# Performance work log

Measured on AMD Instinct MI355X. Metric: run time of the kernel, lower is better.

The kernel has to match this reference:

```python
import jax, jax.numpy as jnp
import numpy as np

N, D, H, E = 50000, 128, 512, 500000

def setup_inputs() -> dict:
    key = jax.random.key(0)
    k1, k2, k3, k4 = jax.random.split(key, 4)
    z = jax.random.normal(k1, (N, D), dtype=jnp.float32)
    edge_index = jax.random.randint(k2, (2, E), 0, N, dtype=jnp.int64)
    # torch Linear weights: fc1 [H, 2D], fc2 [1, H]
    W1 = jax.random.normal(k3, (H, 2 * D), dtype=jnp.float32) * (1.0 / np.sqrt(2 * D))
    b1 = jnp.zeros((H,), dtype=jnp.float32)
    W2 = jax.random.normal(k4, (1, H), dtype=jnp.float32) * (1.0 / np.sqrt(H))
    b2 = jnp.zeros((1,), dtype=jnp.float32)
    return {"z": z, "edge_index": edge_index, "W1": W1, "b1": b1, "W2": W2, "b2": b2}

def reference(z, edge_index, W1, b1, W2, b2):
    # gather endpoints and concat along feature dim: [E, 2D]
    z_cat = jnp.concatenate([z[edge_index[0]], z[edge_index[1]]], axis=1)
    # dropout is identity at eval (drop_rate effectively 0 for the baseline)
    h = jax.nn.relu(jnp.einsum('ef,hf->eh', z_cat, W1) + b1)  # [E, H]
    y = (jnp.einsum('eh,oh->eo', h, W2) + b2).reshape(-1)     # [E]
    return y
```

## Files before the change

kernel.cpp:

```cpp
#include <hip/hip_runtime.h>


typedef __bf16 bf16x8 __attribute__((ext_vector_type(8)));
typedef float f32x4 __attribute__((ext_vector_type(4)));

__device__ __forceinline__ unsigned short f2b(float f) {
    unsigned int u = __float_as_uint(f);
    u = (u + 0x7fffu + ((u >> 16) & 1u)) >> 16;
    return (unsigned short)u;
}

__device__ __forceinline__ void gload_lds16(const unsigned short* g, unsigned short* l) {
    __builtin_amdgcn_global_load_lds(
        (const __attribute__((address_space(1))) unsigned int*)g,
        (__attribute__((address_space(3))) unsigned int*)l, 16, 0, 0);
}

__global__ void prep_kernel(const float* __restrict__ z, const float* __restrict__ W1,
                            const float* __restrict__ b2p,
                            unsigned short* __restrict__ zb, unsigned short* __restrict__ w1s,
                            float* __restrict__ outz, int nz4, int nout4) {
    int stride = gridDim.x * blockDim.x;
    const int nw = 256 * 64;
    const int total = nz4 + nw + nout4;
    const float b2v = b2p[0];
    for (int idx = blockIdx.x * blockDim.x + threadIdx.x; idx < total; idx += stride) {
        if (idx < nz4) {
            float4 v = ((const float4*)z)[idx];
            ushort4 o;
            o.x = f2b(v.x); o.y = f2b(v.y); o.z = f2b(v.z); o.w = f2b(v.w);
            ((ushort4*)zb)[idx] = o;
        } else if (idx < nz4 + nw) {
            int u = idx - nz4;
            int lane = u & 63;
            int blk  = u >> 6;
            int h  = (blk >> 3) * 16 + (lane & 15);
            int kb = (blk & 7) * 32 + (lane >> 4) * 8;
            const float* src = W1 + h * 256 + kb;
            ushort4 o0, o1;
            float4 v0 = *(const float4*)(src);
            float4 v1 = *(const float4*)(src + 4);
            o0.x = f2b(v0.x); o0.y = f2b(v0.y); o0.z = f2b(v0.z); o0.w = f2b(v0.w);
            o1.x = f2b(v1.x); o1.y = f2b(v1.y); o1.z = f2b(v1.z); o1.w = f2b(v1.w);
            ushort4* dst = (ushort4*)(w1s + u * 8);
            dst[0] = o0; dst[1] = o1;
        } else {
            ((float4*)outz)[idx - nz4 - nw] = (float4){b2v, b2v, b2v, b2v};
        }
    }
}

__global__ __launch_bounds__(512, 2)
void edge_mlp_kernel(const int* __restrict__ ei, const unsigned short* __restrict__ zb,
                     const unsigned short* __restrict__ w1s,
                     const float* __restrict__ b1, const float* __restrict__ W2,
                     float* __restrict__ out, int E, int ntiles) {
    __shared__ unsigned short ldsA[2][64 * 256];
    __shared__ float ldsB1[512];

    const int tid  = threadIdx.x;
    const int lane = tid & 63;
    const int w    = tid >> 6;
    const int l15  = lane & 15;
    const int l4   = lane >> 4;
    const int G    = gridDim.x;
    const int t0   = blockIdx.x;
    if (t0 >= ntiles) return;

    ldsB1[tid] = b1[tid];

    uint4 breg[4][8];
    #pragma unroll
    for (int j = 0; j < 4; ++j)
        #pragma unroll
        for (int kc = 0; kc < 8; ++kc)
            breg[j][kc] = *(const uint4*)(w1s + (((w * 4 + j) * 8 + kc) << 9) + lane * 8);

    f32x4 w2v[4];
    #pragma unroll
    for (int j = 0; j < 4; ++j)
        w2v[j] = *(const f32x4*)&W2[w * 64 + j * 16 + l4 * 4];

    const int side = (lane >> 4) & 1;
    const int rsub = lane >> 5;
    const int swz  = l15 & 7;

#define ISSUE_GATHER(BUF)                                                     \
    do {                                                                      \
        _Pragma("unroll")                                                     \
        for (int q_ = 0; q_ < 4; ++q_) {                                      \
            int m_   = w * 8 + q_ * 2 + rsub;                                 \
            int s15_ = l15 ^ (m_ & 7);                                        \
            gload_lds16(zb + (((long)ival[q_]) << 7) + (s15_ << 3),           \
                        &ldsA[BUF][(w * 8 + q_ * 2) << 8]);                   \
        }                                                                     \
    } while (0)

    asm volatile("s_waitcnt vmcnt(0) lgkmcnt(0)" ::: "memory");

    int ival[4];
    #pragma unroll
    for (int q = 0; q < 4; ++q) {
        int e = t0 * 64 + w * 8 + q * 2 + rsub;
        e = (e < E) ? e : (E - 1);
        ival[q] = ei[side * E + e];
    }
    ISSUE_GATHER(0);
    asm volatile("" ::: "memory");
    {
        int t1 = t0 + G;
        #pragma unroll
        for (int q = 0; q < 4; ++q) {
            int e = t1 * 64 + w * 8 + q * 2 + rsub;
            e = (e < E) ? e : (E - 1);
            ival[q] = ei[side * E + e];
        }
    }
    asm volatile("" ::: "memory");
    if (l4 == 0) {
        #pragma unroll
        for (int i = 0; i < 4; ++i)
            atomicAdd(&out[t0 * 64 + i * 16 + l15], 0.0f);
    }

    int cur = 0;
    for (int t = t0; t < ntiles; t += G) {
        asm volatile("s_waitcnt vmcnt(8)" ::: "memory");
        __builtin_amdgcn_s_barrier();
        asm volatile("" ::: "memory");

        const unsigned short* bufc = &ldsA[cur][0];

        f32x4 acc[4][4];
        {
            f32x4 b1t[4];
            #pragma unroll
            for (int j = 0; j < 4; ++j)
                b1t[j] = *(const f32x4*)&ldsB1[w * 64 + j * 16 + l4 * 4];
            #pragma unroll
            for (int i = 0; i < 4; i++)
                #pragma unroll
                for (int j = 0; j < 4; j++) acc[i][j] = b1t[j];
        }

        __builtin_amdgcn_s_setprio(1);
        #pragma unroll
        for (int kc = 0; kc < 4; ++kc) {
            bf16x8 a[4];
            #pragma unroll
            for (int i = 0; i < 4; ++i)
                a[i] = *(const bf16x8*)&bufc[((l15 + 16 * i) << 8) + ((((kc << 2) + l4) ^ swz) << 3)];
            #pragma unroll
            for (int i = 0; i < 4; ++i)
                #pragma unroll
                for (int j = 0; j < 4; ++j)
                    acc[i][j] = __builtin_amdgcn_mfma_f32_16x16x32_bf16(
                        *(const bf16x8*)&breg[j][kc], a[i], acc[i][j], 0, 0, 0);
        }
        __builtin_amdgcn_s_setprio(0);

        ISSUE_GATHER(cur ^ 1);
        asm volatile("" ::: "memory");

        __builtin_amdgcn_s_setprio(1);
        #pragma unroll
        for (int kc = 4; kc < 8; ++kc) {
            bf16x8 a[4];
            #pragma unroll
            for (int i = 0; i < 4; ++i)
                a[i] = *(const bf16x8*)&bufc[((l15 + 16 * i) << 8) + ((((kc << 2) + l4) ^ swz) << 3)];
            #pragma unroll
            for (int i = 0; i < 4; ++i)
                #pragma unroll
                for (int j = 0; j < 4; ++j)
                    acc[i][j] = __builtin_amdgcn_mfma_f32_16x16x32_bf16(
                        *(const bf16x8*)&breg[j][kc], a[i], acc[i][j], 0, 0, 0);
        }
        __builtin_amdgcn_s_setprio(0);

        {
            int tt = t + 2 * G;
            #pragma unroll
            for (int q = 0; q < 4; ++q) {
                int e = tt * 64 + w * 8 + q * 2 + rsub;
                e = (e < E) ? e : (E - 1);
                ival[q] = ei[side * E + e];
            }
        }
        asm volatile("" ::: "memory");

        float s4[4];
        #pragma unroll
        for (int i = 0; i < 4; i++) {
            float s = 0.f;
            #pragma unroll
            for (int j = 0; j < 4; j++)
                #pragma unroll
                for (int r = 0; r < 4; r++)
                    s = fmaf(fmaxf(acc[i][j][r], 0.f), w2v[j][r], s);
            s += __shfl_xor(s, 16);
            s += __shfl_xor(s, 32);
            s4[i] = s;
        }
        #pragma unroll
        for (int i = 0; i < 4; i++) {
            int e = t * 64 + i * 16 + l15;
            if (l4 == 0 && e < E) atomicAdd(&out[e], s4[i]);
        }

        cur ^= 1;
    }
#undef ISSUE_GATHER
}

extern "C" void kernel_launch(void* const* d_in, const int* in_sizes, int n_in,
                              void* d_out, int out_size, void* d_ws, size_t ws_size,
                              hipStream_t stream) {
    const float* z  = (const float*)d_in[0];
    const int*   ei = (const int*)d_in[1];
    const float* W1 = (const float*)d_in[2];
    const float* b1 = (const float*)d_in[3];
    const float* W2 = (const float*)d_in[4];
    const float* b2 = (const float*)d_in[5];
    float* out = (float*)d_out;

    const int E  = in_sizes[1] / 2;
    const int NZ = in_sizes[0];

    unsigned short* zb  = (unsigned short*)d_ws;
    unsigned short* w1s = zb + NZ;

    prep_kernel<<<2048, 256, 0, stream>>>(z, W1, b2, zb, w1s, out, NZ / 4, E / 4);

    const int ntiles = (E + 63) / 64;
    int grid = 256;
    edge_mlp_kernel<<<grid, 512, 0, stream>>>(ei, zb, w1s, b1, W2, out, E, ntiles);
}
```

Before: 182.8 us.

## Fuse bf16 prep pass into edge MLP kernel via cooperative grid sync

```diff
diff --git a/kernel.cpp b/kernel.cpp
--- a/kernel.cpp
+++ b/kernel.cpp
@@ -1,4 +1,7 @@
 #include <hip/hip_runtime.h>
+#include <hip/hip_cooperative_groups.h>
+
+namespace cg = cooperative_groups;
 
 
 typedef __bf16 bf16x8 __attribute__((ext_vector_type(8)));
@@ -16,45 +19,12 @@
         (__attribute__((address_space(3))) unsigned int*)l, 16, 0, 0);
 }
 
-__global__ void prep_kernel(const float* __restrict__ z, const float* __restrict__ W1,
-                            const float* __restrict__ b2p,
-                            unsigned short* __restrict__ zb, unsigned short* __restrict__ w1s,
-                            float* __restrict__ outz, int nz4, int nout4) {
-    int stride = gridDim.x * blockDim.x;
-    const int nw = 256 * 64;
-    const int total = nz4 + nw + nout4;
-    const float b2v = b2p[0];
-    for (int idx = blockIdx.x * blockDim.x + threadIdx.x; idx < total; idx += stride) {
-        if (idx < nz4) {
-            float4 v = ((const float4*)z)[idx];
-            ushort4 o;
-            o.x = f2b(v.x); o.y = f2b(v.y); o.z = f2b(v.z); o.w = f2b(v.w);
-            ((ushort4*)zb)[idx] = o;
-        } else if (idx < nz4 + nw) {
-            int u = idx - nz4;
-            int lane = u & 63;
-            int blk  = u >> 6;
-            int h  = (blk >> 3) * 16 + (lane & 15);
-            int kb = (blk & 7) * 32 + (lane >> 4) * 8;
-            const float* src = W1 + h * 256 + kb;
-            ushort4 o0, o1;
-            float4 v0 = *(const float4*)(src);
-            float4 v1 = *(const float4*)(src + 4);
-            o0.x = f2b(v0.x); o0.y = f2b(v0.y); o0.z = f2b(v0.z); o0.w = f2b(v0.w);
-            o1.x = f2b(v1.x); o1.y = f2b(v1.y); o1.z = f2b(v1.z); o1.w = f2b(v1.w);
-            ushort4* dst = (ushort4*)(w1s + u * 8);
-            dst[0] = o0; dst[1] = o1;
-        } else {
-            ((float4*)outz)[idx - nz4 - nw] = (float4){b2v, b2v, b2v, b2v};
-        }
-    }
-}
-
 __global__ __launch_bounds__(512, 2)
-void edge_mlp_kernel(const int* __restrict__ ei, const unsigned short* __restrict__ zb,
-                     const unsigned short* __restrict__ w1s,
-                     const float* __restrict__ b1, const float* __restrict__ W2,
-                     float* __restrict__ out, int E, int ntiles) {
+void fused_kernel(const float* __restrict__ z, const int* __restrict__ ei,
+                  const float* __restrict__ W1, const float* __restrict__ b1,
+                  const float* __restrict__ W2, const float* __restrict__ b2p,
+                  unsigned short* __restrict__ zb, unsigned short* __restrict__ w1s,
+                  float* __restrict__ out, int E, int NZ, int ntiles) {
     __shared__ unsigned short ldsA[2][64 * 256];
     __shared__ float ldsB1[512];
 
@@ -65,9 +35,42 @@
     const int l4   = lane >> 4;
     const int G    = gridDim.x;
     const int t0   = blockIdx.x;
-    if (t0 >= ntiles) return;
-
-    ldsB1[tid] = b1[tid];
+
+    {
+        const int nz4   = NZ / 4;
+        const int nw    = 256 * 64;
+        const int nout4 = E / 4;
+        const int total = nz4 + nw + nout4;
+        const int stride = G * 512;
+        const float b2v = b2p[0];
+        for (int idx = t0 * 512 + tid; idx < total; idx += stride) {
+            if (idx < nz4) {
+                float4 v = ((const float4*)z)[idx];
+                ushort4 o;
+                o.x = f2b(v.x); o.y = f2b(v.y); o.z = f2b(v.z); o.w = f2b(v.w);
+                ((ushort4*)zb)[idx] = o;
+            } else if (idx < nz4 + nw) {
+                int u = idx - nz4;
+                int ln = u & 63;
+                int blk  = u >> 6;
+                int h  = (blk >> 3) * 16 + (ln & 15);
+                int kb = (blk & 7) * 32 + (ln >> 4) * 8;
+                const float* src = W1 + h * 256 + kb;
+                ushort4 o0, o1;
+                float4 v0 = *(const float4*)(src);
+                float4 v1 = *(const float4*)(src + 4);
+                o0.x = f2b(v0.x); o0.y = f2b(v0.y); o0.z = f2b(v0.z); o0.w = f2b(v0.w);
+                o1.x = f2b(v1.x); o1.y = f2b(v1.y); o1.z = f2b(v1.z); o1.w = f2b(v1.w);
+                ushort4* dst = (ushort4*)(w1s + u * 8);
+                dst[0] = o0; dst[1] = o1;
+            } else {
+                ((float4*)out)[idx - nz4 - nw] = (float4){b2v, b2v, b2v, b2v};
+            }
+        }
+        ldsB1[tid] = b1[tid];
+    }
+
+    cg::this_grid().sync();
 
     uint4 breg[4][8];
     #pragma unroll
@@ -224,15 +227,17 @@
     const float* b2 = (const float*)d_in[5];
     float* out = (float*)d_out;
 
-    const int E  = in_sizes[1] / 2;
-    const int NZ = in_sizes[0];
+    int E  = in_sizes[1] / 2;
+    int NZ = in_sizes[0];
 
     unsigned short* zb  = (unsigned short*)d_ws;
     unsigned short* w1s = zb + NZ;
 
-    prep_kernel<<<2048, 256, 0, stream>>>(z, W1, b2, zb, w1s, out, NZ / 4, E / 4);
-
-    const int ntiles = (E + 63) / 64;
-    int grid = 256;
-    edge_mlp_kernel<<<grid, 512, 0, stream>>>(ei, zb, w1s, b1, W2, out, E, ntiles);
-}
+    int ntiles = (E + 63) / 64;
+
+    void* args[] = { (void*)&z, (void*)&ei, (void*)&W1, (void*)&b1,
+                     (void*)&W2, (void*)&b2, (void*)&zb, (void*)&w1s,
+                     (void*)&out, (void*)&E, (void*)&NZ, (void*)&ntiles };
+    hipLaunchCooperativeKernel((const void*)fused_kernel,
+                               dim3(256), dim3(512), args, 0, stream);
+}
```

Result: slower. 234.4 us (+28.2%).

## Switch edge MLP GEMM from 16x16x32 to 32x32x16 bf16 MFMA tiles

Applied to the files above, without the earlier changes.

```diff
diff --git a/kernel.cpp b/kernel.cpp
--- a/kernel.cpp
+++ b/kernel.cpp
@@ -2,7 +2,8 @@
 
 
 typedef __bf16 bf16x8 __attribute__((ext_vector_type(8)));
-typedef float f32x4 __attribute__((ext_vector_type(4)));
+typedef float f32x4  __attribute__((ext_vector_type(4)));
+typedef float f32x16 __attribute__((ext_vector_type(16)));
 
 __device__ __forceinline__ unsigned short f2b(float f) {
     unsigned int u = __float_as_uint(f);
@@ -34,8 +35,8 @@
             int u = idx - nz4;
             int lane = u & 63;
             int blk  = u >> 6;
-            int h  = (blk >> 3) * 16 + (lane & 15);
-            int kb = (blk & 7) * 32 + (lane >> 4) * 8;
+            int h  = (blk >> 4) * 32 + (lane & 31);
+            int kb = (blk & 15) * 16 + (lane >> 5) * 8;
             const float* src = W1 + h * 256 + kb;
             ushort4 o0, o1;
             float4 v0 = *(const float4*)(src);
@@ -57,39 +58,36 @@
                      float* __restrict__ out, int E, int ntiles) {
     __shared__ unsigned short ldsA[2][64 * 256];
     __shared__ float ldsB1[512];
+    __shared__ float ldsW2[512];
 
     const int tid  = threadIdx.x;
     const int lane = tid & 63;
     const int w    = tid >> 6;
-    const int l15  = lane & 15;
-    const int l4   = lane >> 4;
+    const int l31  = lane & 31;
+    const int hi   = lane >> 5;
     const int G    = gridDim.x;
     const int t0   = blockIdx.x;
     if (t0 >= ntiles) return;
 
     ldsB1[tid] = b1[tid];
-
-    uint4 breg[4][8];
+    ldsW2[tid] = W2[tid];
+
+    uint4 breg[2][16];
     #pragma unroll
-    for (int j = 0; j < 4; ++j)
-        #pragma unroll
-        for (int kc = 0; kc < 8; ++kc)
-            breg[j][kc] = *(const uint4*)(w1s + (((w * 4 + j) * 8 + kc) << 9) + lane * 8);
-
-    f32x4 w2v[4];
-    #pragma unroll
-    for (int j = 0; j < 4; ++j)
-        w2v[j] = *(const f32x4*)&W2[w * 64 + j * 16 + l4 * 4];
+    for (int j = 0; j < 2; ++j)
+        #pragma unroll
+        for (int kst = 0; kst < 16; ++kst)
+            breg[j][kst] = *(const uint4*)(w1s + (((w * 2 + j) * 16 + kst) << 9) + lane * 8);
 
     const int side = (lane >> 4) & 1;
-    const int rsub = lane >> 5;
-    const int swz  = l15 & 7;
+    const int l15  = lane & 15;
+    const int swz3 = (l31 & 7) << 3;
 
 #define ISSUE_GATHER(BUF)                                                     \
     do {                                                                      \
         _Pragma("unroll")                                                     \
         for (int q_ = 0; q_ < 4; ++q_) {                                      \
-            int m_   = w * 8 + q_ * 2 + rsub;                                 \
+            int m_   = w * 8 + q_ * 2 + hi;                                   \
             int s15_ = l15 ^ (m_ & 7);                                        \
             gload_lds16(zb + (((long)ival[q_]) << 7) + (s15_ << 3),           \
                         &ldsA[BUF][(w * 8 + q_ * 2) << 8]);                   \
@@ -101,7 +99,7 @@
     int ival[4];
     #pragma unroll
     for (int q = 0; q < 4; ++q) {
-        int e = t0 * 64 + w * 8 + q * 2 + rsub;
+        int e = t0 * 64 + w * 8 + q * 2 + hi;
         e = (e < E) ? e : (E - 1);
         ival[q] = ei[side * E + e];
     }
@@ -111,51 +109,54 @@
         int t1 = t0 + G;
         #pragma unroll
         for (int q = 0; q < 4; ++q) {
-            int e = t1 * 64 + w * 8 + q * 2 + rsub;
+            int e = t1 * 64 + w * 8 + q * 2 + hi;
             e = (e < E) ? e : (E - 1);
             ival[q] = ei[side * E + e];
         }
     }
     asm volatile("" ::: "memory");
-    if (l4 == 0) {
-        #pragma unroll
-        for (int i = 0; i < 4; ++i)
-            atomicAdd(&out[t0 * 64 + i * 16 + l15], 0.0f);
+    if (hi == 0) {
+        atomicAdd(&out[t0 * 64 + l31], 0.0f);
+        atomicAdd(&out[t0 * 64 + 32 + l31], 0.0f);
     }
 
     int cur = 0;
     for (int t = t0; t < ntiles; t += G) {
-        asm volatile("s_waitcnt vmcnt(8)" ::: "memory");
+        asm volatile("s_waitcnt vmcnt(6)" ::: "memory");
         __builtin_amdgcn_s_barrier();
         asm volatile("" ::: "memory");
 
         const unsigned short* bufc = &ldsA[cur][0];
 
-        f32x4 acc[4][4];
-        {
-            f32x4 b1t[4];
-            #pragma unroll
-            for (int j = 0; j < 4; ++j)
-                b1t[j] = *(const f32x4*)&ldsB1[w * 64 + j * 16 + l4 * 4];
-            #pragma unroll
-            for (int i = 0; i < 4; i++)
-                #pragma unroll
-                for (int j = 0; j < 4; j++) acc[i][j] = b1t[j];
-        }
+        f32x16 acc[2][2];
+        #pragma unroll
+        for (int j = 0; j < 2; ++j)
+            #pragma unroll
+            for (int q = 0; q < 4; ++q) {
+                f32x4 b = *(const f32x4*)&ldsB1[w * 64 + j * 32 + q * 8 + hi * 4];
+                #pragma unroll
+                for (int rr = 0; rr < 4; ++rr) {
+                    acc[0][j][q * 4 + rr] = b[rr];
+                    acc[1][j][q * 4 + rr] = b[rr];
+                }
+            }
 
         __builtin_amdgcn_s_setprio(1);
         #pragma unroll
-        for (int kc = 0; kc < 4; ++kc) {
-            bf16x8 a[4];
-            #pragma unroll
-            for (int i = 0; i < 4; ++i)
-                a[i] = *(const bf16x8*)&bufc[((l15 + 16 * i) << 8) + ((((kc << 2) + l4) ^ swz) << 3)];
-            #pragma unroll
-            for (int i = 0; i < 4; ++i)
-                #pragma unroll
-                for (int j = 0; j < 4; ++j)
-                    acc[i][j] = __builtin_amdgcn_mfma_f32_16x16x32_bf16(
-                        *(const bf16x8*)&breg[j][kc], a[i], acc[i][j], 0, 0, 0);
+        for (int kst = 0; kst < 8; ++kst) {
+            bf16x8 a[2];
+            #pragma unroll
+            for (int i = 0; i < 2; ++i) {
+                int s = kst * 2 + hi;
+                int off = ((i * 32 + l31) << 8) + ((s & 16) << 3) + (((s & 15) << 3) ^ swz3);
+                a[i] = *(const bf16x8*)&bufc[off];
+            }
+            #pragma unroll
+            for (int i = 0; i < 2; ++i)
+                #pragma unroll
+                for (int j = 0; j < 2; ++j)
+                    acc[i][j] = __builtin_amdgcn_mfma_f32_32x32x16_bf16(
+                        *(const bf16x8*)&breg[j][kst], a[i], acc[i][j], 0, 0, 0);
         }
         __builtin_amdgcn_s_setprio(0);
 
@@ -164,17 +165,20 @@
 
         __builtin_amdgcn_s_setprio(1);
         #pragma unroll
-        for (int kc = 4; kc < 8; ++kc) {
-            bf16x8 a[4];
-            #pragma unroll
-            for (int i = 0; i < 4; ++i)
-                a[i] = *(const bf16x8*)&bufc[((l15 + 16 * i) << 8) + ((((kc << 2) + l4) ^ swz) << 3)];
-            #pragma unroll
-            for (int i = 0; i < 4; ++i)
-                #pragma unroll
-                for (int j = 0; j < 4; ++j)
-                    acc[i][j] = __builtin_amdgcn_mfma_f32_16x16x32_bf16(
-                        *(const bf16x8*)&breg[j][kc], a[i], acc[i][j], 0, 0, 0);
+        for (int kst = 8; kst < 16; ++kst) {
+            bf16x8 a[2];
+            #pragma unroll
+            for (int i = 0; i < 2; ++i) {
+                int s = kst * 2 + hi;
+                int off = ((i * 32 + l31) << 8) + ((s & 16) << 3) + (((s & 15) << 3) ^ swz3);
+                a[i] = *(const bf16x8*)&bufc[off];
+            }
+            #pragma unroll
+            for (int i = 0; i < 2; ++i)
+                #pragma unroll
+                for (int j = 0; j < 2; ++j)
+                    acc[i][j] = __builtin_amdgcn_mfma_f32_32x32x16_bf16(
+                        *(const bf16x8*)&breg[j][kst], a[i], acc[i][j], 0, 0, 0);
         }
         __builtin_amdgcn_s_setprio(0);
 
@@ -182,30 +186,33 @@
             int tt = t + 2 * G;
             #pragma unroll
             for (int q = 0; q < 4; ++q) {
-                int e = tt * 64 + w * 8 + q * 2 + rsub;
+                int e = tt * 64 + w * 8 + q * 2 + hi;
                 e = (e < E) ? e : (E - 1);
                 ival[q] = ei[side * E + e];
             }
         }
         asm volatile("" ::: "memory");
 
-        float s4[4];
-        #pragma unroll
-        for (int i = 0; i < 4; i++) {
+        float s2[2];
+        #pragma unroll
+        for (int i = 0; i < 2; ++i) {
             float s = 0.f;
             #pragma unroll
-            for (int j = 0; j < 4; j++)
-                #pragma unroll
-                for (int r = 0; r < 4; r++)
-                    s = fmaf(fmaxf(acc[i][j][r], 0.f), w2v[j][r], s);
-            s += __shfl_xor(s, 16);
+            for (int j = 0; j < 2; ++j)
+                #pragma unroll
+                for (int q = 0; q < 4; ++q) {
+                    f32x4 w2q = *(const f32x4*)&ldsW2[w * 64 + j * 32 + q * 8 + hi * 4];
+                    #pragma unroll
+                    for (int rr = 0; rr < 4; ++rr)
+                        s = fmaf(fmaxf(acc[i][j][q * 4 + rr], 0.f), w2q[rr], s);
+                }
             s += __shfl_xor(s, 32);
-            s4[i] = s;
-        }
-        #pragma unroll
-        for (int i = 0; i < 4; i++) {
-            int e = t * 64 + i * 16 + l15;
-            if (l4 == 0 && e < E) atomicAdd(&out[e], s4[i]);
+            s2[i] = s;
+        }
+        #pragma unroll
+        for (int i = 0; i < 2; ++i) {
+            int e = t * 64 + i * 32 + l31;
+            if (hi == 0 && e < E) atomicAdd(&out[e], s2[i]);
         }
 
         cur ^= 1;
```

New measurement: 190.5 us. 1.04x slower.
